# Optimization experiments

Measured on AMD Instinct MI355X. Metric: run time of the kernel, lower is better.

## Reference

```python
import jax, jax.numpy as jnp
import numpy as np

EPS_ALPHA = 1e-7
EPS_STEP = 1e-6


def setup_inputs() -> dict:
    key = jax.random.key(0)
    k1, k2, k3 = jax.random.split(key, 3)
    B, T, D = 32, 1024, 512
    x = jax.random.normal(k1, (B, T, D), dtype=jnp.float32)
    # Linear(in_dim, 1) params (sigmoid-gain init approximated with small normal)
    W = jax.random.normal(k2, (D, 1), dtype=jnp.float32) * (1.0 / np.sqrt(D))
    b = jnp.zeros((1,), dtype=jnp.float32)
    return {"x": x, "W": W, "b": b, "r": 1, "num_steps": 1024}


def reference(x, W, b, r, num_steps):
    # x: [B, T, D]; r is unused (as in the original forward)
    B, T, D = x.shape
    speeds = jax.nn.sigmoid(jnp.einsum('btd,do->bto', x, W) + b)  # [B, T, 1]
    sp = speeds[:, :, 0]  # [B, T]

    # alpha0 = [1, 1e-7, 1e-7, ...]
    alpha0 = jnp.concatenate(
        [jnp.ones((B, 1), x.dtype), jnp.full((B, T - 1), EPS_ALPHA, x.dtype)], axis=1)

    def step(alpha, _):
        # u = alpha . speeds  -> [B, 1]
        u = jnp.sum(alpha * sp, axis=1, keepdims=True)
        sq = 1.7 - jnp.abs(u - 0.5)  # 1 + 0.7 - |u-0.5|
        shifted = jnp.pad(alpha[:, :-1], ((0, 0), (1, 0)))  # forward shift
        a = ((1.0 - u) * alpha + u * shifted + EPS_STEP) ** sq
        a = a / jnp.sum(a, axis=1, keepdims=True)
        return a, a

    _, alphas = jax.lax.scan(step, alpha0, None, length=num_steps)  # [S, B, T]
    alphas = jnp.transpose(alphas, (1, 0, 2))  # [B, S, T]
    contexts = jnp.einsum('bst,btd->bsd', alphas, x)  # [B, S, D]
    return contexts, alphas
```

## Files before the change

kernel.cpp:

```cpp
#include <hip/hip_runtime.h>
#include <hip/hip_bf16.h>

#define NB 32
#define NT 1024
#define ND 512
#define NS 1024

#define CTX_ELEMS (32u * 1024u * 512u)
#define SP_SCRATCH_OFF (CTX_ELEMS - 32u*1024u)

__device__ __forceinline__ float vlog2(float x) {
    float r; asm("v_log_f32 %0, %1" : "=v"(r) : "v"(x)); return r;
}
__device__ __forceinline__ float vexp2(float x) {
    float r; asm("v_exp_f32 %0, %1" : "=v"(r) : "v"(x)); return r;
}
__device__ __forceinline__ float vrcp(float x) {
    float r; asm("v_rcp_f32 %0, %1" : "=v"(r) : "v"(x)); return r;
}

template<int ctrl, int rm, int bm, bool bc>
__device__ __forceinline__ float dppadd(float x) {
    int y = __builtin_amdgcn_update_dpp(0, __float_as_int(x), ctrl, rm, bm, bc);
    return x + __int_as_float(y);
}
__device__ __forceinline__ float reduce63(float x) {
    x = dppadd<0x111, 0xf, 0xf, true >(x);
    x = dppadd<0x112, 0xf, 0xf, true >(x);
    x = dppadd<0x114, 0xf, 0xf, true >(x);
    x = dppadd<0x118, 0xf, 0xf, true >(x);
    x = dppadd<0x142, 0xa, 0xf, false>(x);
    x = dppadd<0x143, 0xc, 0xf, false>(x);
    return x;
}
__device__ __forceinline__ float wave_shr1(float x) {
    int y = __builtin_amdgcn_update_dpp(0, __float_as_int(x), 0x138, 0xf, 0xf, true);
    return __int_as_float(y);
}

__device__ __forceinline__ void lds_barrier() {
    asm volatile("s_waitcnt lgkmcnt(0)" ::: "memory");
    __builtin_amdgcn_s_barrier();
    asm volatile("" ::: "memory");
}

__global__ __launch_bounds__(256) void sp_kernel(const float* __restrict__ x,
                                                 const float* __restrict__ W,
                                                 const float* __restrict__ bias,
                                                 float* __restrict__ sp)
{
    const int lane = threadIdx.x & 63;
    const int wid  = threadIdx.x >> 6;
    const int row  = blockIdx.x * 4 + wid;
    const float4* xr = reinterpret_cast<const float4*>(x + (size_t)row * ND) + lane * 2;
    const float4* wr = reinterpret_cast<const float4*>(W) + lane * 2;
    float4 xa = xr[0], xb = xr[1];
    float4 wa = wr[0], wb = wr[1];
    float d = xa.x*wa.x + xa.y*wa.y + xa.z*wa.z + xa.w*wa.w
            + xb.x*wb.x + xb.y*wb.y + xb.z*wb.z + xb.w*wb.w;
    #pragma unroll
    for (int m = 1; m < 64; m <<= 1) d += __shfl_xor(d, m);
    if (lane == 0) {
        float z = d + bias[0];
        float e = vexp2(-z * 1.442695040888963f);
        sp[row] = 1.0f / (1.0f + e);
    }
}

__global__ __launch_bounds__(256) void scan_kernel(const float* __restrict__ sp,
                                                   float* __restrict__ alphas)
{
    const int b    = blockIdx.x;
    const int tx   = threadIdx.x;
    const int lane = tx & 63;
    const int wid  = tx >> 6;

    __shared__ float r1[2][4];
    __shared__ float r2[2][4];
    __shared__ float rb[2][4];

    float spv[4], raw[4];
    {
        float4 v = *reinterpret_cast<const float4*>(sp + (size_t)b * NT + tx * 4);
        spv[0] = v.x; spv[1] = v.y; spv[2] = v.z; spv[3] = v.w;
    }
    #pragma unroll
    for (int j = 0; j < 4; ++j) raw[j] = 1e-7f;
    if (tx == 0) raw[0] = 1.0f;
    float carry = (wid == 0) ? 0.0f : 1e-7f;

    {
        float p2 = fmaf(raw[0], spv[0], fmaf(raw[1], spv[1], fmaf(raw[2], spv[2], raw[3]*spv[3])));
        p2 = reduce63(p2);
        if (lane == 63) r2[1][wid] = p2;
    }
    lds_barrier();
    float u;
    {
        float4 v2 = *reinterpret_cast<const float4*>(r2[1]);
        u = (v2.x + v2.y) + (v2.z + v2.w);
    }
    float inv = 1.0f;

    float* outp = alphas + (size_t)b * NS * NT + tx * 4;

    for (int s = 0; s < NS; ++s) {
        const int p = s & 1;
        const float sq = 1.7f - fabsf(u - 0.5f);
        const float c1 = (1.0f - u) * inv;
        const float c0 = u * inv;

        float prev = wave_shr1(raw[3]);
        float sh0  = (lane == 0) ? carry : prev;

        float anew[4];
        {
            float v0 = fmaf(c1, raw[0], fmaf(c0, sh0,    1e-6f));
            float v1 = fmaf(c1, raw[1], fmaf(c0, raw[0], 1e-6f));
            float v2 = fmaf(c1, raw[2], fmaf(c0, raw[1], 1e-6f));
            float v3 = fmaf(c1, raw[3], fmaf(c0, raw[2], 1e-6f));
            anew[0] = vexp2(sq * vlog2(v0));
            anew[1] = vexp2(sq * vlog2(v1));
            anew[2] = vexp2(sq * vlog2(v2));
            anew[3] = vexp2(sq * vlog2(v3));
        }

        float p1 = (anew[0] + anew[1]) + (anew[2] + anew[3]);
        float p2 = fmaf(anew[0], spv[0], anew[1]*spv[1]) + fmaf(anew[2], spv[2], anew[3]*spv[3]);
        p1 = reduce63(p1);
        p2 = reduce63(p2);
        if (lane == 63) { r1[p][wid] = p1; r2[p][wid] = p2; rb[p][wid] = anew[3]; }
        lds_barrier();

        float4 v1 = *reinterpret_cast<const float4*>(r1[p]);
        float4 v2 = *reinterpret_cast<const float4*>(r2[p]);
        float bc  = rb[p][(wid == 0) ? 0 : (wid - 1)];
        carry = (wid == 0) ? 0.0f : bc;

        float t1 = (v1.x + v1.y) + (v1.z + v1.w);
        float t2 = (v2.x + v2.y) + (v2.z + v2.w);
        inv = vrcp(t1);
        u   = t2 * inv;

        float4 o;
        o.x = anew[0] * inv; o.y = anew[1] * inv; o.z = anew[2] * inv; o.w = anew[3] * inv;
        *reinterpret_cast<float4*>(outp + (size_t)s * NT) = o;

        #pragma unroll
        for (int j = 0; j < 4; ++j) raw[j] = anew[j];
    }
}

typedef __bf16 bf16x8 __attribute__((ext_vector_type(8)));
typedef float  f32x4  __attribute__((ext_vector_type(4)));

#define BM 256
#define BN 256
#define BK 32
#define LDP 40

__global__ __launch_bounds__(512, 2) void gemm_kernel(const float* __restrict__ alphas,
                                                      const float* __restrict__ x,
                                                      float* __restrict__ contexts)
{
    __shared__ __align__(16) __bf16 As[BM * LDP];
    __shared__ __align__(16) __bf16 Xs[BN * LDP];

    const int b  = blockIdx.z;
    const int s0 = blockIdx.y * BM;
    const int n0 = blockIdx.x * BN;
    const int tx = threadIdx.x;
    const int lane = tx & 63;
    const int wid  = tx >> 6;
    const int wm = wid >> 2;
    const int wn = wid & 3;
    const int lr = lane & 15;
    const int lk = (lane >> 4) * 8;

    f32x4 acc[8][4];
    #pragma unroll
    for (int i = 0; i < 8; ++i)
        #pragma unroll
        for (int j = 0; j < 4; ++j) acc[i][j] = (f32x4){0.f, 0.f, 0.f, 0.f};

    const int arow = tx >> 1;
    const int akb  = (tx & 1) * 16;
    const int xk0 = tx >> 6;
    const int xn4 = (tx & 63) * 4;

    const float* ap = alphas + ((size_t)b * NS + s0 + arow) * NT + akb;
    const float* xp = x + ((size_t)b * NT + xk0) * ND + n0 + xn4;

    float4 va0 = reinterpret_cast<const float4*>(ap)[0];
    float4 va1 = reinterpret_cast<const float4*>(ap)[1];
    float4 va2 = reinterpret_cast<const float4*>(ap)[2];
    float4 va3 = reinterpret_cast<const float4*>(ap)[3];
    float4 vx0 = *reinterpret_cast<const float4*>(xp + 0 * 8 * ND);
    float4 vx1 = *reinterpret_cast<const float4*>(xp + 1 * 8 * ND);
    float4 vx2 = *reinterpret_cast<const float4*>(xp + 2 * 8 * ND);
    float4 vx3 = *reinterpret_cast<const float4*>(xp + 3 * 8 * ND);
    ap += BK;
    xp += (size_t)BK * ND;

    for (int k0 = 0; k0 < NT; k0 += BK) {
        {
            bf16x8 w0, w1;
            w0[0]=(__bf16)va0.x; w0[1]=(__bf16)va0.y; w0[2]=(__bf16)va0.z; w0[3]=(__bf16)va0.w;
            w0[4]=(__bf16)va1.x; w0[5]=(__bf16)va1.y; w0[6]=(__bf16)va1.z; w0[7]=(__bf16)va1.w;
            w1[0]=(__bf16)va2.x; w1[1]=(__bf16)va2.y; w1[2]=(__bf16)va2.z; w1[3]=(__bf16)va2.w;
            w1[4]=(__bf16)va3.x; w1[5]=(__bf16)va3.y; w1[6]=(__bf16)va3.z; w1[7]=(__bf16)va3.w;
            *reinterpret_cast<bf16x8*>(&As[arow * LDP + akb])     = w0;
            *reinterpret_cast<bf16x8*>(&As[arow * LDP + akb + 8]) = w1;
            Xs[(xn4+0)*LDP + xk0]      = (__bf16)vx0.x;
            Xs[(xn4+1)*LDP + xk0]      = (__bf16)vx0.y;
            Xs[(xn4+2)*LDP + xk0]      = (__bf16)vx0.z;
            Xs[(xn4+3)*LDP + xk0]      = (__bf16)vx0.w;
            Xs[(xn4+0)*LDP + xk0 + 8]  = (__bf16)vx1.x;
            Xs[(xn4+1)*LDP + xk0 + 8]  = (__bf16)vx1.y;
            Xs[(xn4+2)*LDP + xk0 + 8]  = (__bf16)vx1.z;
            Xs[(xn4+3)*LDP + xk0 + 8]  = (__bf16)vx1.w;
            Xs[(xn4+0)*LDP + xk0 + 16] = (__bf16)vx2.x;
            Xs[(xn4+1)*LDP + xk0 + 16] = (__bf16)vx2.y;
            Xs[(xn4+2)*LDP + xk0 + 16] = (__bf16)vx2.z;
            Xs[(xn4+3)*LDP + xk0 + 16] = (__bf16)vx2.w;
            Xs[(xn4+0)*LDP + xk0 + 24] = (__bf16)vx3.x;
            Xs[(xn4+1)*LDP + xk0 + 24] = (__bf16)vx3.y;
            Xs[(xn4+2)*LDP + xk0 + 24] = (__bf16)vx3.z;
            Xs[(xn4+3)*LDP + xk0 + 24] = (__bf16)vx3.w;
        }
        if (k0 + BK < NT) {
            va0 = reinterpret_cast<const float4*>(ap)[0];
            va1 = reinterpret_cast<const float4*>(ap)[1];
            va2 = reinterpret_cast<const float4*>(ap)[2];
            va3 = reinterpret_cast<const float4*>(ap)[3];
            vx0 = *reinterpret_cast<const float4*>(xp + 0 * 8 * ND);
            vx1 = *reinterpret_cast<const float4*>(xp + 1 * 8 * ND);
            vx2 = *reinterpret_cast<const float4*>(xp + 2 * 8 * ND);
            vx3 = *reinterpret_cast<const float4*>(xp + 3 * 8 * ND);
            ap += BK;
            xp += (size_t)BK * ND;
        }
        lds_barrier();

        bf16x8 av[8], bv[4];
        #pragma unroll
        for (int j = 0; j < 4; ++j)
            bv[j] = *reinterpret_cast<const bf16x8*>(&Xs[(wn*64 + j*16 + lr) * LDP + lk]);
        #pragma unroll
        for (int i = 0; i < 8; ++i)
            av[i] = *reinterpret_cast<const bf16x8*>(&As[(wm*128 + i*16 + lr) * LDP + lk]);
        #pragma unroll
        for (int i = 0; i < 8; ++i)
            #pragma unroll
            for (int j = 0; j < 4; ++j)
                acc[i][j] = __builtin_amdgcn_mfma_f32_16x16x32_bf16(av[i], bv[j], acc[i][j], 0, 0, 0);
        lds_barrier();
    }

    const int ccol = lr;
    const int crow = (lane >> 4) * 4;
    #pragma unroll
    for (int i = 0; i < 8; ++i) {
        #pragma unroll
        for (int j = 0; j < 4; ++j) {
            int col = n0 + wn*64 + j*16 + ccol;
            int rw  = s0 + wm*128 + i*16 + crow;
            #pragma unroll
            for (int r = 0; r < 4; ++r)
                contexts[((size_t)b * NS + rw + r) * ND + col] = acc[i][j][r];
        }
    }
}

extern "C" void kernel_launch(void* const* d_in, const int* in_sizes, int n_in,
                              void* d_out, int out_size, void* d_ws, size_t ws_size,
                              hipStream_t stream) {
    const float* x    = (const float*)d_in[0];
    const float* W    = (const float*)d_in[1];
    const float* bias = (const float*)d_in[2];
    float* contexts = (float*)d_out;
    float* alphas   = (float*)d_out + CTX_ELEMS;
    float* sp       = (float*)d_out + SP_SCRATCH_OFF;

    sp_kernel<<<dim3(NB * NT / 4), dim3(256), 0, stream>>>(x, W, bias, sp);
    scan_kernel<<<dim3(NB), dim3(256), 0, stream>>>(sp, alphas);
    gemm_kernel<<<dim3(ND / BN, NS / BM, NB), dim3(512), 0, stream>>>(alphas, x, contexts);
}
```

Before: 400.2 us.

## Interleave two batch scans per block to hide barrier latency

Each scan block now processes two batch rows, software-pipelining them. One row's element computation and reductions run while the other row waits on its LDS barrier. This is meant to hide the per-step sync and reduction latency of the serial 1024-step recurrence. The cost is half as many blocks (16 instead of 32 CUs used), more registers, and longer per-step work per block.

```diff
diff --git a/kernel.cpp b/kernel.cpp
--- a/kernel.cpp
+++ b/kernel.cpp
@@ -67,87 +67,133 @@
     }
 }
 
+
+#define ELEM(raw, spv, carry, u, inv, an, P1, P2, BND) do {                          \
+    float sq_ = 1.7f - fabsf((u) - 0.5f);                                            \
+    float c1_ = (1.0f - (u)) * (inv);                                                \
+    float c0_ = (u) * (inv);                                                         \
+    float prev_ = wave_shr1(raw[3]);                                                 \
+    float sh_ = (lane == 0) ? (carry) : prev_;                                       \
+    an[0] = vexp2(sq_ * vlog2(fmaf(c1_, raw[0], fmaf(c0_, sh_,    1e-6f))));         \
+    an[1] = vexp2(sq_ * vlog2(fmaf(c1_, raw[1], fmaf(c0_, raw[0], 1e-6f))));         \
+    an[2] = vexp2(sq_ * vlog2(fmaf(c1_, raw[2], fmaf(c0_, raw[1], 1e-6f))));         \
+    an[3] = vexp2(sq_ * vlog2(fmaf(c1_, raw[3], fmaf(c0_, raw[2], 1e-6f))));         \
+    P1 = (an[0] + an[1]) + (an[2] + an[3]);                                          \
+    P2 = fmaf(an[0], spv[0], an[1]*spv[1]) + fmaf(an[2], spv[2], an[3]*spv[3]);      \
+    P1 = reduce63(P1);                                                               \
+    P2 = reduce63(P2);                                                               \
+    BND = an[3];                                                                     \
+} while (0)
+
 __global__ __launch_bounds__(256) void scan_kernel(const float* __restrict__ sp,
                                                    float* __restrict__ alphas)
 {
-    const int b    = blockIdx.x;
+    const int bA   = blockIdx.x * 2;
+    const int bB   = bA + 1;
     const int tx   = threadIdx.x;
     const int lane = tx & 63;
     const int wid  = tx >> 6;
 
-    __shared__ float r1[2][4];
-    __shared__ float r2[2][4];
-    __shared__ float rb[2][4];
-
-    float spv[4], raw[4];
+    __shared__ __align__(16) float r1A[2][4], r2A[2][4], rbA[2][4];
+    __shared__ __align__(16) float r1B[2][4], r2B[2][4], rbB[2][4];
+
+    float spA[4], spB[4], rawA[4], rawB[4];
     {
-        float4 v = *reinterpret_cast<const float4*>(sp + (size_t)b * NT + tx * 4);
-        spv[0] = v.x; spv[1] = v.y; spv[2] = v.z; spv[3] = v.w;
+        float4 v = *reinterpret_cast<const float4*>(sp + (size_t)bA * NT + tx * 4);
+        spA[0]=v.x; spA[1]=v.y; spA[2]=v.z; spA[3]=v.w;
+        float4 w = *reinterpret_cast<const float4*>(sp + (size_t)bB * NT + tx * 4);
+        spB[0]=w.x; spB[1]=w.y; spB[2]=w.z; spB[3]=w.w;
     }
     #pragma unroll
-    for (int j = 0; j < 4; ++j) raw[j] = 1e-7f;
-    if (tx == 0) raw[0] = 1.0f;
-    float carry = (wid == 0) ? 0.0f : 1e-7f;
+    for (int j = 0; j < 4; ++j) { rawA[j] = 1e-7f; rawB[j] = 1e-7f; }
+    if (tx == 0) { rawA[0] = 1.0f; rawB[0] = 1.0f; }
+    float carryA = (wid == 0) ? 0.0f : 1e-7f;
+    float carryB = carryA;
 
     {
-        float p2 = fmaf(raw[0], spv[0], fmaf(raw[1], spv[1], fmaf(raw[2], spv[2], raw[3]*spv[3])));
-        p2 = reduce63(p2);
-        if (lane == 63) r2[1][wid] = p2;
+        float qA = fmaf(rawA[0], spA[0], fmaf(rawA[1], spA[1], fmaf(rawA[2], spA[2], rawA[3]*spA[3])));
+        float qB = fmaf(rawB[0], spB[0], fmaf(rawB[1], spB[1], fmaf(rawB[2], spB[2], rawB[3]*spB[3])));
+        qA = reduce63(qA);
+        qB = reduce63(qB);
+        if (lane == 63) { r2A[1][wid] = qA; r2B[1][wid] = qB; }
     }
     lds_barrier();
-    float u;
+    float uA, uB;
     {
-        float4 v2 = *reinterpret_cast<const float4*>(r2[1]);
-        u = (v2.x + v2.y) + (v2.z + v2.w);
-    }
-    float inv = 1.0f;
-
-    float* outp = alphas + (size_t)b * NS * NT + tx * 4;
+        float4 vA = *reinterpret_cast<const float4*>(r2A[1]);
+        float4 vB = *reinterpret_cast<const float4*>(r2B[1]);
+        uA = (vA.x + vA.y) + (vA.z + vA.w);
+        uB = (vB.x + vB.y) + (vB.z + vB.w);
+    }
+    float invA = 1.0f, invB = 1.0f;
+
+    float anA[4], anB[4];
+    float p1A, p2A, bndA, p1B, p2B, bndB;
+    ELEM(rawA, spA, carryA, uA, invA, anA, p1A, p2A, bndA);
+
+    float* outA = alphas + (size_t)bA * NS * NT + tx * 4;
+    float* outB = alphas + (size_t)bB * NS * NT + tx * 4;
 
     for (int s = 0; s < NS; ++s) {
         const int p = s & 1;
-        const float sq = 1.7f - fabsf(u - 0.5f);
-        const float c1 = (1.0f - u) * inv;
-        const float c0 = u * inv;
-
-        float prev = wave_shr1(raw[3]);
-        float sh0  = (lane == 0) ? carry : prev;
-
-        float anew[4];
+
+        if (lane == 63) { r1A[p][wid] = p1A; r2A[p][wid] = p2A; rbA[p][wid] = bndA; }
+
+        ELEM(rawB, spB, carryB, uB, invB, anB, p1B, p2B, bndB);
+
+        if (s) {
+            float4 o;
+            o.x = rawA[0]*invA; o.y = rawA[1]*invA; o.z = rawA[2]*invA; o.w = rawA[3]*invA;
+            *reinterpret_cast<float4*>(outA) = o;
+            outA += NT;
+        }
+        lds_barrier();
+
         {
-            float v0 = fmaf(c1, raw[0], fmaf(c0, sh0,    1e-6f));
-            float v1 = fmaf(c1, raw[1], fmaf(c0, raw[0], 1e-6f));
-            float v2 = fmaf(c1, raw[2], fmaf(c0, raw[1], 1e-6f));
-            float v3 = fmaf(c1, raw[3], fmaf(c0, raw[2], 1e-6f));
-            anew[0] = vexp2(sq * vlog2(v0));
-            anew[1] = vexp2(sq * vlog2(v1));
-            anew[2] = vexp2(sq * vlog2(v2));
-            anew[3] = vexp2(sq * vlog2(v3));
-        }
-
-        float p1 = (anew[0] + anew[1]) + (anew[2] + anew[3]);
-        float p2 = fmaf(anew[0], spv[0], anew[1]*spv[1]) + fmaf(anew[2], spv[2], anew[3]*spv[3]);
-        p1 = reduce63(p1);
-        p2 = reduce63(p2);
-        if (lane == 63) { r1[p][wid] = p1; r2[p][wid] = p2; rb[p][wid] = anew[3]; }
+            float4 v1 = *reinterpret_cast<const float4*>(r1A[p]);
+            float4 v2 = *reinterpret_cast<const float4*>(r2A[p]);
+            float bc  = rbA[p][(wid == 0) ? 0 : (wid - 1)];
+            carryA = (wid == 0) ? 0.0f : bc;
+            float t1 = (v1.x + v1.y) + (v1.z + v1.w);
+            float t2 = (v2.x + v2.y) + (v2.z + v2.w);
+            invA = vrcp(t1);
+            uA   = t2 * invA;
+        }
+        #pragma unroll
+        for (int j = 0; j < 4; ++j) rawA[j] = anA[j];
+
+        if (lane == 63) { r1B[p][wid] = p1B; r2B[p][wid] = p2B; rbB[p][wid] = bndB; }
+
+        ELEM(rawA, spA, carryA, uA, invA, anA, p1A, p2A, bndA);
+
+        if (s) {
+            float4 o;
+            o.x = rawB[0]*invB; o.y = rawB[1]*invB; o.z = rawB[2]*invB; o.w = rawB[3]*invB;
+            *reinterpret_cast<float4*>(outB) = o;
+            outB += NT;
+        }
         lds_barrier();
 
-        float4 v1 = *reinterpret_cast<const float4*>(r1[p]);
-        float4 v2 = *reinterpret_cast<const float4*>(r2[p]);
-        float bc  = rb[p][(wid == 0) ? 0 : (wid - 1)];
-        carry = (wid == 0) ? 0.0f : bc;
-
-        float t1 = (v1.x + v1.y) + (v1.z + v1.w);
-        float t2 = (v2.x + v2.y) + (v2.z + v2.w);
-        inv = vrcp(t1);
-        u   = t2 * inv;
-
+        {
+            float4 v1 = *reinterpret_cast<const float4*>(r1B[p]);
+            float4 v2 = *reinterpret_cast<const float4*>(r2B[p]);
+            float bc  = rbB[p][(wid == 0) ? 0 : (wid - 1)];
+            carryB = (wid == 0) ? 0.0f : bc;
+            float t1 = (v1.x + v1.y) + (v1.z + v1.w);
+            float t2 = (v2.x + v2.y) + (v2.z + v2.w);
+            invB = vrcp(t1);
+            uB   = t2 * invB;
+        }
+        #pragma unroll
+        for (int j = 0; j < 4; ++j) rawB[j] = anB[j];
+    }
+
+    {
         float4 o;
-        o.x = anew[0] * inv; o.y = anew[1] * inv; o.z = anew[2] * inv; o.w = anew[3] * inv;
-        *reinterpret_cast<float4*>(outp + (size_t)s * NT) = o;
-
-        #pragma unroll
-        for (int j = 0; j < 4; ++j) raw[j] = anew[j];
+        o.x = rawA[0]*invA; o.y = rawA[1]*invA; o.z = rawA[2]*invA; o.w = rawA[3]*invA;
+        *reinterpret_cast<float4*>(outA) = o;
+        o.x = rawB[0]*invB; o.y = rawB[1]*invB; o.z = rawB[2]*invB; o.w = rawB[3]*invB;
+        *reinterpret_cast<float4*>(outB) = o;
     }
 }
 
@@ -283,6 +329,6 @@
     float* sp       = (float*)d_out + SP_SCRATCH_OFF;
 
     sp_kernel<<<dim3(NB * NT / 4), dim3(256), 0, stream>>>(x, W, bias, sp);
-    scan_kernel<<<dim3(NB), dim3(256), 0, stream>>>(sp, alphas);
+    scan_kernel<<<dim3(NB / 2), dim3(256), 0, stream>>>(sp, alphas);
     gemm_kernel<<<dim3(ND / BN, NS / BM, NB), dim3(512), 0, stream>>>(alphas, x, contexts);
 }
```

After: 775.2 us. +93.7%, slower.

## Run scan with a single wave per batch row, removing LDS barriers

Applied to the files above, without the earlier changes.

Rewrites the sequential alpha scan to use one 64-lane wave per batch row, with each lane handling 16 elements instead of 4. Cross-segment boundary values and reductions use readlane instead of LDS writes plus a workgroup barrier each step. The loop is unrolled by two with ping-pong register arrays. This trades four times more per-wave transcendental work for removing per-step barrier and LDS latency on the serial critical path.

```diff
diff --git a/kernel.cpp b/kernel.cpp
--- a/kernel.cpp
+++ b/kernel.cpp
@@ -36,6 +36,9 @@
 __device__ __forceinline__ float wave_shr1(float x) {
     int y = __builtin_amdgcn_update_dpp(0, __float_as_int(x), 0x138, 0xf, 0xf, true);
     return __int_as_float(y);
+}
+__device__ __forceinline__ float rdlane63(float x) {
+    return __int_as_float(__builtin_amdgcn_readlane(__float_as_int(x), 63));
 }
 
 __device__ __forceinline__ void lds_barrier() {
@@ -67,87 +70,104 @@
     }
 }
 
-__global__ __launch_bounds__(256) void scan_kernel(const float* __restrict__ sp,
-                                                   float* __restrict__ alphas)
+
+#define EROW(RAW, AN, j, SH0)                                                          \
+    AN[j][0] = vexp2(sq * vlog2(fmaf(c1, RAW[j][0], fmaf(c0, SH0,       1e-6f))));     \
+    AN[j][1] = vexp2(sq * vlog2(fmaf(c1, RAW[j][1], fmaf(c0, RAW[j][0], 1e-6f))));     \
+    AN[j][2] = vexp2(sq * vlog2(fmaf(c1, RAW[j][2], fmaf(c0, RAW[j][1], 1e-6f))));     \
+    AN[j][3] = vexp2(sq * vlog2(fmaf(c1, RAW[j][3], fmaf(c0, RAW[j][2], 1e-6f))));
+
+#define STEP(RAW, AN)                                                                  \
+    do {                                                                               \
+        const float sq = 1.7f - fabsf(u - 0.5f);                                       \
+        const float c1 = (1.0f - u) * inv;                                             \
+        const float c0 = u * inv;                                                      \
+        float bndA = rdlane63(RAW[0][3]);                                              \
+        float bndB = rdlane63(RAW[1][3]);                                              \
+        float bndC = rdlane63(RAW[2][3]);                                              \
+        float pr0 = wave_shr1(RAW[0][3]);                                              \
+        float pr1 = wave_shr1(RAW[1][3]);                                              \
+        float pr2 = wave_shr1(RAW[2][3]);                                              \
+        float pr3 = wave_shr1(RAW[3][3]);                                              \
+        float sh0 = (lane == 0) ? 0.0f : pr0;                                          \
+        float sh1 = (lane == 0) ? bndA : pr1;                                          \
+        float sh2 = (lane == 0) ? bndB : pr2;                                          \
+        float sh3 = (lane == 0) ? bndC : pr3;                                          \
+        EROW(RAW, AN, 0, sh0)                                                          \
+        EROW(RAW, AN, 1, sh1)                                                          \
+        EROW(RAW, AN, 2, sh2)                                                          \
+        EROW(RAW, AN, 3, sh3)                                                          \
+        float s0 = (AN[0][0] + AN[0][1]) + (AN[0][2] + AN[0][3]);                      \
+        float s1 = (AN[1][0] + AN[1][1]) + (AN[1][2] + AN[1][3]);                      \
+        float s2 = (AN[2][0] + AN[2][1]) + (AN[2][2] + AN[2][3]);                      \
+        float s3 = (AN[3][0] + AN[3][1]) + (AN[3][2] + AN[3][3]);                      \
+        float q0 = fmaf(AN[0][0], spv[0][0], AN[0][1]*spv[0][1])                       \
+                 + fmaf(AN[0][2], spv[0][2], AN[0][3]*spv[0][3]);                      \
+        float q1 = fmaf(AN[1][0], spv[1][0], AN[1][1]*spv[1][1])                       \
+                 + fmaf(AN[1][2], spv[1][2], AN[1][3]*spv[1][3]);                      \
+        float q2 = fmaf(AN[2][0], spv[2][0], AN[2][1]*spv[2][1])                       \
+                 + fmaf(AN[2][2], spv[2][2], AN[2][3]*spv[2][3]);                      \
+        float q3 = fmaf(AN[3][0], spv[3][0], AN[3][1]*spv[3][1])                       \
+                 + fmaf(AN[3][2], spv[3][2], AN[3][3]*spv[3][3]);                      \
+        float p1 = (s0 + s1) + (s2 + s3);                                              \
+        float p2 = (q0 + q1) + (q2 + q3);                                              \
+        p1 = reduce63(p1);                                                             \
+        p2 = reduce63(p2);                                                             \
+        float t1 = rdlane63(p1);                                                       \
+        float t2 = rdlane63(p2);                                                       \
+        inv = vrcp(t1);                                                                \
+        u   = t2 * inv;                                                                \
+        float4 o;                                                                      \
+        o.x = AN[0][0]*inv; o.y = AN[0][1]*inv; o.z = AN[0][2]*inv; o.w = AN[0][3]*inv;\
+        *reinterpret_cast<float4*>(outp + 0*256) = o;                                  \
+        o.x = AN[1][0]*inv; o.y = AN[1][1]*inv; o.z = AN[1][2]*inv; o.w = AN[1][3]*inv;\
+        *reinterpret_cast<float4*>(outp + 1*256) = o;                                  \
+        o.x = AN[2][0]*inv; o.y = AN[2][1]*inv; o.z = AN[2][2]*inv; o.w = AN[2][3]*inv;\
+        *reinterpret_cast<float4*>(outp + 2*256) = o;                                  \
+        o.x = AN[3][0]*inv; o.y = AN[3][1]*inv; o.z = AN[3][2]*inv; o.w = AN[3][3]*inv;\
+        *reinterpret_cast<float4*>(outp + 3*256) = o;                                  \
+        outp += NT;                                                                    \
+    } while (0)
+
+__global__ __launch_bounds__(64) void scan_kernel(const float* __restrict__ sp,
+                                                  float* __restrict__ alphas)
 {
     const int b    = blockIdx.x;
-    const int tx   = threadIdx.x;
-    const int lane = tx & 63;
-    const int wid  = tx >> 6;
-
-    __shared__ float r1[2][4];
-    __shared__ float r2[2][4];
-    __shared__ float rb[2][4];
-
-    float spv[4], raw[4];
-    {
-        float4 v = *reinterpret_cast<const float4*>(sp + (size_t)b * NT + tx * 4);
-        spv[0] = v.x; spv[1] = v.y; spv[2] = v.z; spv[3] = v.w;
-    }
-    #pragma unroll
-    for (int j = 0; j < 4; ++j) raw[j] = 1e-7f;
-    if (tx == 0) raw[0] = 1.0f;
-    float carry = (wid == 0) ? 0.0f : 1e-7f;
-
-    {
-        float p2 = fmaf(raw[0], spv[0], fmaf(raw[1], spv[1], fmaf(raw[2], spv[2], raw[3]*spv[3])));
-        p2 = reduce63(p2);
-        if (lane == 63) r2[1][wid] = p2;
-    }
-    lds_barrier();
+    const int lane = threadIdx.x;
+
+    float spv[4][4], raw[4][4], an[4][4];
+    #pragma unroll
+    for (int j = 0; j < 4; ++j) {
+        float4 v = *reinterpret_cast<const float4*>(sp + (size_t)b * NT + j * 256 + lane * 4);
+        spv[j][0] = v.x; spv[j][1] = v.y; spv[j][2] = v.z; spv[j][3] = v.w;
+    }
+    #pragma unroll
+    for (int j = 0; j < 4; ++j)
+        #pragma unroll
+        for (int c = 0; c < 4; ++c) raw[j][c] = 1e-7f;
+    if (lane == 0) raw[0][0] = 1.0f;
+
     float u;
     {
-        float4 v2 = *reinterpret_cast<const float4*>(r2[1]);
-        u = (v2.x + v2.y) + (v2.z + v2.w);
+        float q0 = fmaf(raw[0][0], spv[0][0], raw[0][1]*spv[0][1])
+                 + fmaf(raw[0][2], spv[0][2], raw[0][3]*spv[0][3]);
+        float q1 = fmaf(raw[1][0], spv[1][0], raw[1][1]*spv[1][1])
+                 + fmaf(raw[1][2], spv[1][2], raw[1][3]*spv[1][3]);
+        float q2 = fmaf(raw[2][0], spv[2][0], raw[2][1]*spv[2][1])
+                 + fmaf(raw[2][2], spv[2][2], raw[2][3]*spv[2][3]);
+        float q3 = fmaf(raw[3][0], spv[3][0], raw[3][1]*spv[3][1])
+                 + fmaf(raw[3][2], spv[3][2], raw[3][3]*spv[3][3]);
+        float p2 = (q0 + q1) + (q2 + q3);
+        p2 = reduce63(p2);
+        u = rdlane63(p2);
     }
     float inv = 1.0f;
 
-    float* outp = alphas + (size_t)b * NS * NT + tx * 4;
-
-    for (int s = 0; s < NS; ++s) {
-        const int p = s & 1;
-        const float sq = 1.7f - fabsf(u - 0.5f);
-        const float c1 = (1.0f - u) * inv;
-        const float c0 = u * inv;
-
-        float prev = wave_shr1(raw[3]);
-        float sh0  = (lane == 0) ? carry : prev;
-
-        float anew[4];
-        {
-            float v0 = fmaf(c1, raw[0], fmaf(c0, sh0,    1e-6f));
-            float v1 = fmaf(c1, raw[1], fmaf(c0, raw[0], 1e-6f));
-            float v2 = fmaf(c1, raw[2], fmaf(c0, raw[1], 1e-6f));
-            float v3 = fmaf(c1, raw[3], fmaf(c0, raw[2], 1e-6f));
-            anew[0] = vexp2(sq * vlog2(v0));
-            anew[1] = vexp2(sq * vlog2(v1));
-            anew[2] = vexp2(sq * vlog2(v2));
-            anew[3] = vexp2(sq * vlog2(v3));
-        }
-
-        float p1 = (anew[0] + anew[1]) + (anew[2] + anew[3]);
-        float p2 = fmaf(anew[0], spv[0], anew[1]*spv[1]) + fmaf(anew[2], spv[2], anew[3]*spv[3]);
-        p1 = reduce63(p1);
-        p2 = reduce63(p2);
-        if (lane == 63) { r1[p][wid] = p1; r2[p][wid] = p2; rb[p][wid] = anew[3]; }
-        lds_barrier();
-
-        float4 v1 = *reinterpret_cast<const float4*>(r1[p]);
-        float4 v2 = *reinterpret_cast<const float4*>(r2[p]);
-        float bc  = rb[p][(wid == 0) ? 0 : (wid - 1)];
-        carry = (wid == 0) ? 0.0f : bc;
-
-        float t1 = (v1.x + v1.y) + (v1.z + v1.w);
-        float t2 = (v2.x + v2.y) + (v2.z + v2.w);
-        inv = vrcp(t1);
-        u   = t2 * inv;
-
-        float4 o;
-        o.x = anew[0] * inv; o.y = anew[1] * inv; o.z = anew[2] * inv; o.w = anew[3] * inv;
-        *reinterpret_cast<float4*>(outp + (size_t)s * NT) = o;
-
-        #pragma unroll
-        for (int j = 0; j < 4; ++j) raw[j] = anew[j];
+    float* outp = alphas + (size_t)b * NS * NT + lane * 4;
+
+    for (int s = 0; s < NS; s += 2) {
+        STEP(raw, an);
+        STEP(an, raw);
     }
 }
 
@@ -283,6 +303,6 @@
     float* sp       = (float*)d_out + SP_SCRATCH_OFF;
 
     sp_kernel<<<dim3(NB * NT / 4), dim3(256), 0, stream>>>(x, W, bias, sp);
-    scan_kernel<<<dim3(NB), dim3(256), 0, stream>>>(sp, alphas);
+    scan_kernel<<<dim3(NB), dim3(64), 0, stream>>>(sp, alphas);
     gemm_kernel<<<dim3(ND / BN, NS / BM, NB), dim3(512), 0, stream>>>(alphas, x, contexts);
 }
```

New measurement: 545.4 us. 1.36x slower.

## Widen scan to 512 threads and remap GEMM blocks for XCD locality

Applied to the files above, without the earlier changes.

The scan kernel now uses 8 waves per batch row, each thread holding 2 elements instead of 4. This halves the per-step serial transcendental work per thread, at the cost of a wider cross-wave reduction through shared memory. The GEMM launch becomes a 1D grid with a block-index swizzle. The swizzle places the two N-halves of the same (batch, s-block) pair on the same low-3-bit slot, likely so they land on the same XCD and share alpha tiles in L2.

```diff
diff --git a/kernel.cpp b/kernel.cpp
--- a/kernel.cpp
+++ b/kernel.cpp
@@ -67,7 +67,7 @@
     }
 }
 
-__global__ __launch_bounds__(256) void scan_kernel(const float* __restrict__ sp,
+__global__ __launch_bounds__(512) void scan_kernel(const float* __restrict__ sp,
                                                    float* __restrict__ alphas)
 {
     const int b    = blockIdx.x;
@@ -75,34 +75,34 @@
     const int lane = tx & 63;
     const int wid  = tx >> 6;
 
-    __shared__ float r1[2][4];
-    __shared__ float r2[2][4];
-    __shared__ float rb[2][4];
-
-    float spv[4], raw[4];
+    __shared__ __align__(16) float r1[2][8];
+    __shared__ __align__(16) float r2[2][8];
+    __shared__ __align__(16) float rb[2][8];
+
+    float spv[2], raw[2];
     {
-        float4 v = *reinterpret_cast<const float4*>(sp + (size_t)b * NT + tx * 4);
-        spv[0] = v.x; spv[1] = v.y; spv[2] = v.z; spv[3] = v.w;
-    }
-    #pragma unroll
-    for (int j = 0; j < 4; ++j) raw[j] = 1e-7f;
+        float2 v = *reinterpret_cast<const float2*>(sp + (size_t)b * NT + tx * 2);
+        spv[0] = v.x; spv[1] = v.y;
+    }
+    raw[0] = 1e-7f; raw[1] = 1e-7f;
     if (tx == 0) raw[0] = 1.0f;
     float carry = (wid == 0) ? 0.0f : 1e-7f;
 
     {
-        float p2 = fmaf(raw[0], spv[0], fmaf(raw[1], spv[1], fmaf(raw[2], spv[2], raw[3]*spv[3])));
-        p2 = reduce63(p2);
-        if (lane == 63) r2[1][wid] = p2;
+        float q = fmaf(raw[0], spv[0], raw[1] * spv[1]);
+        q = reduce63(q);
+        if (lane == 63) r2[1][wid] = q;
     }
     lds_barrier();
     float u;
     {
-        float4 v2 = *reinterpret_cast<const float4*>(r2[1]);
-        u = (v2.x + v2.y) + (v2.z + v2.w);
+        float4 a = *reinterpret_cast<const float4*>(&r2[1][0]);
+        float4 c = *reinterpret_cast<const float4*>(&r2[1][4]);
+        u = ((a.x + a.y) + (a.z + a.w)) + ((c.x + c.y) + (c.z + c.w));
     }
     float inv = 1.0f;
 
-    float* outp = alphas + (size_t)b * NS * NT + tx * 4;
+    float* outp = alphas + (size_t)b * NS * NT + tx * 2;
 
     for (int s = 0; s < NS; ++s) {
         const int p = s & 1;
@@ -110,44 +110,36 @@
         const float c1 = (1.0f - u) * inv;
         const float c0 = u * inv;
 
-        float prev = wave_shr1(raw[3]);
+        float prev = wave_shr1(raw[1]);
         float sh0  = (lane == 0) ? carry : prev;
 
-        float anew[4];
-        {
-            float v0 = fmaf(c1, raw[0], fmaf(c0, sh0,    1e-6f));
-            float v1 = fmaf(c1, raw[1], fmaf(c0, raw[0], 1e-6f));
-            float v2 = fmaf(c1, raw[2], fmaf(c0, raw[1], 1e-6f));
-            float v3 = fmaf(c1, raw[3], fmaf(c0, raw[2], 1e-6f));
-            anew[0] = vexp2(sq * vlog2(v0));
-            anew[1] = vexp2(sq * vlog2(v1));
-            anew[2] = vexp2(sq * vlog2(v2));
-            anew[3] = vexp2(sq * vlog2(v3));
-        }
-
-        float p1 = (anew[0] + anew[1]) + (anew[2] + anew[3]);
-        float p2 = fmaf(anew[0], spv[0], anew[1]*spv[1]) + fmaf(anew[2], spv[2], anew[3]*spv[3]);
+        float an0 = vexp2(sq * vlog2(fmaf(c1, raw[0], fmaf(c0, sh0,    1e-6f))));
+        float an1 = vexp2(sq * vlog2(fmaf(c1, raw[1], fmaf(c0, raw[0], 1e-6f))));
+
+        float p1 = an0 + an1;
+        float p2 = fmaf(an0, spv[0], an1 * spv[1]);
         p1 = reduce63(p1);
         p2 = reduce63(p2);
-        if (lane == 63) { r1[p][wid] = p1; r2[p][wid] = p2; rb[p][wid] = anew[3]; }
+        if (lane == 63) { r1[p][wid] = p1; r2[p][wid] = p2; rb[p][wid] = an1; }
         lds_barrier();
 
-        float4 v1 = *reinterpret_cast<const float4*>(r1[p]);
-        float4 v2 = *reinterpret_cast<const float4*>(r2[p]);
-        float bc  = rb[p][(wid == 0) ? 0 : (wid - 1)];
+        float4 a = *reinterpret_cast<const float4*>(&r1[p][0]);
+        float4 bq = *reinterpret_cast<const float4*>(&r1[p][4]);
+        float4 c = *reinterpret_cast<const float4*>(&r2[p][0]);
+        float4 d = *reinterpret_cast<const float4*>(&r2[p][4]);
+        float bc = rb[p][(wid == 0) ? 0 : (wid - 1)];
         carry = (wid == 0) ? 0.0f : bc;
 
-        float t1 = (v1.x + v1.y) + (v1.z + v1.w);
-        float t2 = (v2.x + v2.y) + (v2.z + v2.w);
+        float t1 = ((a.x + a.y) + (a.z + a.w)) + ((bq.x + bq.y) + (bq.z + bq.w));
+        float t2 = ((c.x + c.y) + (c.z + c.w)) + ((d.x + d.y) + (d.z + d.w));
         inv = vrcp(t1);
         u   = t2 * inv;
 
-        float4 o;
-        o.x = anew[0] * inv; o.y = anew[1] * inv; o.z = anew[2] * inv; o.w = anew[3] * inv;
-        *reinterpret_cast<float4*>(outp + (size_t)s * NT) = o;
-
-        #pragma unroll
-        for (int j = 0; j < 4; ++j) raw[j] = anew[j];
+        float2 o;
+        o.x = an0 * inv; o.y = an1 * inv;
+        *reinterpret_cast<float2*>(outp + (size_t)s * NT) = o;
+
+        raw[0] = an0; raw[1] = an1;
     }
 }
 
@@ -166,9 +158,16 @@
     __shared__ __align__(16) __bf16 As[BM * LDP];
     __shared__ __align__(16) __bf16 Xs[BN * LDP];
 
-    const int b  = blockIdx.z;
-    const int s0 = blockIdx.y * BM;
-    const int n0 = blockIdx.x * BN;
+    const int bid  = blockIdx.x;
+    const int low3 = bid & 7;
+    const int slot = bid >> 3;
+    const int nb   = slot & 1;
+    const int pair = (slot >> 1) * 8 + low3;
+    const int b    = pair >> 2;
+    const int sbi  = pair & 3;
+    const int s0 = sbi * BM;
+    const int n0 = nb * BN;
+
     const int tx = threadIdx.x;
     const int lane = tx & 63;
     const int wid  = tx >> 6;
@@ -283,6 +282,6 @@
     float* sp       = (float*)d_out + SP_SCRATCH_OFF;
 
     sp_kernel<<<dim3(NB * NT / 4), dim3(256), 0, stream>>>(x, W, bias, sp);
-    scan_kernel<<<dim3(NB), dim3(256), 0, stream>>>(sp, alphas);
-    gemm_kernel<<<dim3(ND / BN, NS / BM, NB), dim3(512), 0, stream>>>(alphas, x, contexts);
-}
+    scan_kernel<<<dim3(NB), dim3(512), 0, stream>>>(sp, alphas);
+    gemm_kernel<<<dim3(256), dim3(512), 0, stream>>>(alphas, x, contexts);
+}
```

Result: slower. 477.6 us (+19.3%).
